# Kernel optimization log

Hardware: AMD Instinct MI355X
Metric: run time of the kernel (lower is better)

Reference implementation:

```python
import jax, jax.numpy as jnp
import numpy as np

DIM = 192          # out_dim
HEADS = 8          # num_heads (split into 2 branches of 4)
SS = (4, 8)        # split_size
B, HH, WW, CIN = 8, 128, 128, 192


def calc_mask(H, W, wh, ww):
    # Swin-style shift mask for windows of (wh, ww), shift (wh//2, ww//2).
    sh, sw = wh // 2, ww // 2
    h = jnp.arange(H)
    w = jnp.arange(W)
    hreg = (h >= H - wh).astype(jnp.int32) + (h >= H - sh).astype(jnp.int32)
    wreg = (w >= W - ww).astype(jnp.int32) + (w >= W - sw).astype(jnp.int32)
    img = hreg[:, None] * 3 + wreg[None, :]                      # (H, W) region ids
    win = img.reshape(H // wh, wh, W // ww, ww).transpose(0, 2, 1, 3).reshape(-1, wh * ww)
    return jnp.where(win[:, :, None] != win[:, None, :], -100.0, 0.0)  # (nW, N, N)


def window_attention(q, k, v, mask, d, Hsp, Wsp):
    # q,k,v: (B, C, H, W); mask: (u*v, N, N); d heads, window Hsp x Wsp
    Bc, C, H, W = k.shape
    u, vv = H // Hsp, W // Wsp
    c = C // d
    N = Hsp * Wsp
    scale = c ** -0.5

    def v2w(t):  # 'b (d c) (u h) (v w) -> (b u v) d (h w) c'
        return t.reshape(Bc, d, c, u, Hsp, vv, Wsp).transpose(0, 3, 5, 1, 4, 6, 2).reshape(Bc * u * vv, d, N, c)

    qw, kw, vw = v2w(q), v2w(k), v2w(v)
    attn = jnp.einsum('ndic,ndjc->ndij', qw, kw) * scale          # (B*u*v, d, N, N)
    attn = attn.reshape(Bc, u * vv, d, N, N) + mask[None, :, None, :, :]
    a = jax.nn.softmax(attn, axis=-1).reshape(Bc * u * vv, d, N, N)
    o = jnp.einsum('ndij,ndjc->ndic', a, vw)
    # '(b u v) d (h w) c -> b (d c) (u h) (v w)'
    return o.reshape(Bc, u, vv, d, Hsp, Wsp, c).transpose(0, 3, 6, 1, 4, 2, 5).reshape(Bc, C, H, W)


def setup_inputs() -> dict:
    key = jax.random.key(0)
    k0, k1, k2, k3 = jax.random.split(key, 4)
    x = jax.random.normal(k0, (B, HH * WW, CIN), dtype=jnp.float32)
    Wq = jax.random.normal(k1, (CIN, DIM), dtype=jnp.float32) * 0.02
    Wkv = jax.random.normal(k2, (CIN, 2 * DIM), dtype=jnp.float32) * 0.02
    Wproj = jax.random.normal(k3, (DIM, DIM), dtype=jnp.float32) * 0.02
    bproj = jnp.zeros((DIM,), dtype=jnp.float32)
    return {"x": x, "Wq": Wq, "Wkv": Wkv, "Wproj": Wproj, "bproj": bproj, "H": HH, "W": WW}


def reference(x, Wq, Wkv, Wproj, bproj, H, W):
    Bc, L, _ = x.shape
    C = Wq.shape[1]
    q = (x @ Wq).reshape(Bc, H, W, C).transpose(0, 3, 1, 2)       # (B, C, H, W)
    kv = (x @ Wkv).reshape(Bc, H, W, 2, C)
    k = kv[..., 0, :].transpose(0, 3, 1, 2)
    v = kv[..., 1, :].transpose(0, 3, 1, 2)

    Ch = C // 2
    s0, s1 = SS[0] // 2, SS[1] // 2
    roll0 = lambda t: jnp.roll(t, (-s0, -s1), axis=(-2, -1))
    roll1 = lambda t: jnp.roll(t, (-s1, -s0), axis=(-2, -1))
    mask0 = calc_mask(H, W, SS[0], SS[1])   # branch 0: 4x8 windows
    mask1 = calc_mask(H, W, SS[1], SS[0])   # branch 1: 8x4 windows
    d = HEADS // 2

    x0 = window_attention(roll0(q[:, :Ch]), roll0(k[:, :Ch]), roll0(v[:, :Ch]), mask0, d, SS[0], SS[1])
    x1 = window_attention(roll1(q[:, Ch:]), roll1(k[:, Ch:]), roll1(v[:, Ch:]), mask1, d, SS[1], SS[0])
    x0 = jnp.roll(x0, (s0, s1), axis=(-2, -1))
    x1 = jnp.roll(x1, (s1, s0), axis=(-2, -1))

    out = jnp.concatenate([x0, x1], axis=1)                        # (B, C, H, W)
    out = out.transpose(0, 2, 3, 1).reshape(Bc, L, C)
    return out @ Wproj + bproj
```

## Files before the change

### kernel.cpp

```cpp
#include <hip/hip_runtime.h>
#include <hip/hip_bf16.h>
#include <stdint.h>

typedef __bf16 bf16;
typedef __bf16 bf16x8 __attribute__((ext_vector_type(8)));
typedef __bf16 bf16x4 __attribute__((ext_vector_type(4)));
typedef float  f32x4  __attribute__((ext_vector_type(4)));

#define MROWS 131072

__device__ __forceinline__ f32x4 mfma16(bf16x8 a, bf16x8 b, f32x4 c) {
    return __builtin_amdgcn_mfma_f32_16x16x32_bf16(a, b, c, 0, 0, 0);
}
__device__ __forceinline__ f32x4 zero4() {
    f32x4 z; z[0]=0.f; z[1]=0.f; z[2]=0.f; z[3]=0.f; return z;
}
__device__ __forceinline__ bf16x8 zero8() {
    bf16x8 z;
#pragma unroll
    for (int i = 0; i < 8; ++i) z[i] = (bf16)0.f;
    return z;
}
template <int CTRL>
__device__ __forceinline__ float rowror(float x) {
    return __int_as_float(
        __builtin_amdgcn_mov_dpp(__float_as_int(x), CTRL, 0xF, 0xF, false));
}
__device__ __forceinline__ float rowmax16(float m) {
    m = fmaxf(m, rowror<0x128>(m));
    m = fmaxf(m, rowror<0x124>(m));
    m = fmaxf(m, rowror<0x122>(m));
    m = fmaxf(m, rowror<0x121>(m));
    return m;
}
__device__ __forceinline__ float rowsum16(float s) {
    s += rowror<0x128>(s);
    s += rowror<0x124>(s);
    s += rowror<0x122>(s);
    s += rowror<0x121>(s);
    return s;
}

__global__ void kw_transpose(const float* __restrict__ Wq, const float* __restrict__ Wkv,
                             const float* __restrict__ Wp, bf16* __restrict__ Wt,
                             bf16* __restrict__ Wpt) {
    int col = blockIdx.x;
    int k = threadIdx.x;
    if (col < 192)      Wt[col * 192 + k] = (bf16)Wq[k * 192 + col];
    else if (col < 576) Wt[col * 192 + k] = (bf16)Wkv[k * 384 + (col - 192)];
    else                Wpt[(col - 576) * 192 + k] = (bf16)Wp[k * 192 + (col - 576)];
}

__global__ __launch_bounds__(256, 4) void kfused(const float* __restrict__ X,
                                                 const bf16* __restrict__ Wt,
                                                 bf16* __restrict__ Out) {
    const int bid = blockIdx.x;
    const int slab = bid & 7;
    const int t = bid >> 3;
    const int img = t >> 7;
    const int idx = t & 127;
    int branch, wa, wb;
    if (idx < 64) {
        branch = 0; wa = slab * 4 + (idx >> 4); wb = idx & 15;
    } else {
        branch = 1; int j = idx - 64; wa = slab * 2 + (j >> 5); wb = j & 31;
    }
    const int wh = branch ? 8 : 4, ww = branch ? 4 : 8;
    const int lww = branch ? 2 : 3;
    const int sh = wh >> 1, sw = ww >> 1;

    __shared__ __align__(16) char smem[31232];
    bf16 (*xs)[200]    = (bf16(*)[200])smem;
    bf16 (*qs)[104]    = (bf16(*)[104])smem;
    bf16 (*ob)[104]    = (bf16(*)[104])smem;
    bf16 (*kss)[104]   = (bf16(*)[104])(smem + 6656);
    bf16 (*pl)[32][40] = (bf16(*)[32][40])(smem + 13312);
    bf16 (*vt)[24][40] = (bf16(*)[24][40])(smem + 23552);
    __shared__ int pix[32];
    __shared__ int rid[32];

    const int tid = threadIdx.x;
    const int hd = tid >> 6;
    const int l = tid & 63, li = l & 15, lk = l >> 4;

    if (tid < 32) {
        int ih = tid >> lww, iw = tid & (ww - 1);
        int hh = wa * wh + ih, wp = wb * ww + iw;
        int hreg = (hh >= 128 - wh) + (hh >= 128 - sh);
        int wreg = (wp >= 128 - ww) + (wp >= 128 - sw);
        rid[tid] = hreg * 3 + wreg;
        int srh = (hh + sh) & 127, srw = (wp + sw) & 127;
        pix[tid] = img * 16384 + srh * 128 + srw;
    }

#pragma unroll
    for (int i = 0; i < 3; ++i) {
        int c = tid + i * 256;
        int row = c / 24, col8 = (c % 24) * 8;
        int ih = row >> lww, iw = row & (ww - 1);
        int hh = wa * wh + ih, wp = wb * ww + iw;
        int srh = (hh + sh) & 127, srw = (wp + sw) & 127;
        const float* p = X + (size_t)(img * 16384 + srh * 128 + srw) * 192 + col8;
        f32x4 f0 = *(const f32x4*)p;
        f32x4 f1 = *(const f32x4*)(p + 4);
        bf16x8 v;
#pragma unroll
        for (int e = 0; e < 4; ++e) { v[e] = (bf16)f0[e]; v[4 + e] = (bf16)f1[e]; }
        *(bf16x8*)&xs[row][col8] = v;
    }
    __syncthreads();

    bf16x8 xf[2][6];
#pragma unroll
    for (int mt = 0; mt < 2; ++mt)
#pragma unroll
        for (int ks = 0; ks < 6; ++ks)
            xf[mt][ks] = *(const bf16x8*)&xs[mt * 16 + li][ks * 32 + lk * 8];

#define LOADW(dst, nt) {                                                            \
        int seg_ = (nt) / 6, cwi_ = ((nt) % 6) * 16;                                \
        const bf16* wr = Wt + (size_t)(seg_ * 192 + branch * 96 + cwi_ + li) * 192  \
                            + lk * 8;                                               \
        _Pragma("unroll")                                                           \
        for (int ks = 0; ks < 6; ++ks) dst[ks] = *(const bf16x8*)(wr + ks * 32);    \
    }
#define MFMA_SCATTER(frag, nt) {                                                    \
        f32x4 a0 = zero4(), a1 = zero4();                                           \
        _Pragma("unroll")                                                           \
        for (int ks = 0; ks < 6; ++ks) {                                            \
            a0 = mfma16(frag[ks], xf[0][ks], a0);                                   \
            a1 = mfma16(frag[ks], xf[1][ks], a1);                                   \
        }                                                                           \
        int seg_ = (nt) / 6, cwi_ = ((nt) % 6) * 16;                                \
        if (seg_ < 2) {                                                             \
            bf16 (*dst)[104] = (seg_ == 0) ? qs : kss;                              \
            bf16x4 p0, p1;                                                          \
            _Pragma("unroll")                                                       \
            for (int r = 0; r < 4; ++r) { p0[r] = (bf16)a0[r]; p1[r] = (bf16)a1[r]; } \
            *(bf16x4*)&dst[li][cwi_ + lk * 4] = p0;                                 \
            *(bf16x4*)&dst[16 + li][cwi_ + lk * 4] = p1;                            \
        } else {                                                                    \
            _Pragma("unroll")                                                       \
            for (int r = 0; r < 4; ++r) {                                           \
                int vc = cwi_ + lk * 4 + r;                                         \
                vt[vc / 24][vc % 24][li] = (bf16)a0[r];                             \
                vt[vc / 24][vc % 24][16 + li] = (bf16)a1[r];                        \
            }                                                                       \
        }                                                                           \
    }

    bf16x8 cur[6], nxt[6];
    LOADW(cur, hd);
    __syncthreads();

#pragma unroll
    for (int j = 0; j < 4; ++j) {
        int nt = hd + 4 * j;
        if (j < 3) {
            LOADW(nxt, nt + 4);
        } else if (hd < 2) {
            LOADW(nxt, nt + 4);
        }
        MFMA_SCATTER(cur, nt);
#pragma unroll
        for (int ks = 0; ks < 6; ++ks) cur[ks] = nxt[ks];
    }
    if (hd < 2) {
        MFMA_SCATTER(cur, hd + 16);
    }
    __syncthreads();

    bf16x8 aq[2], bk[2];
#pragma unroll
    for (int t2 = 0; t2 < 2; ++t2) {
        if (lk < 3) {
            aq[t2] = *(const bf16x8*)&qs[t2 * 16 + li][hd * 24 + lk * 8];
            bk[t2] = *(const bf16x8*)&kss[t2 * 16 + li][hd * 24 + lk * 8];
        } else {
            aq[t2] = zero8();
            bk[t2] = zero8();
        }
    }
    f32x4 s[2][2];
#pragma unroll
    for (int it = 0; it < 2; ++it)
#pragma unroll
        for (int jt = 0; jt < 2; ++jt) s[it][jt] = mfma16(aq[it], bk[jt], zero4());

    const float scale = 0.2041241452319315f;
    const int r0 = lk * 4;
    const int rj0 = rid[li], rj1 = rid[16 + li];
#pragma unroll
    for (int it = 0; it < 2; ++it) {
#pragma unroll
        for (int r = 0; r < 4; ++r) {
            int i = it * 16 + r0 + r;
            int ri = rid[i];
            float v0 = s[it][0][r] * scale + ((ri != rj0) ? -100.f : 0.f);
            float v1 = s[it][1][r] * scale + ((ri != rj1) ? -100.f : 0.f);
            float m = rowmax16(fmaxf(v0, v1));
            float e0 = __expf(v0 - m), e1 = __expf(v1 - m);
            float sm = rowsum16(e0 + e1);
            float inv = 1.f / sm;
            pl[hd][i][li] = (bf16)(e0 * inv);
            pl[hd][i][16 + li] = (bf16)(e1 * inv);
        }
    }
    __syncthreads();

    bf16x8 ap[2], bv[2];
#pragma unroll
    for (int it = 0; it < 2; ++it)
        ap[it] = *(const bf16x8*)&pl[hd][it * 16 + li][lk * 8];
#pragma unroll
    for (int ct = 0; ct < 2; ++ct) {
        int col = ct * 16 + li;
        if (col > 23) col = 23;
        bv[ct] = *(const bf16x8*)&vt[hd][col][lk * 8];
    }
    f32x4 o[2][2];
#pragma unroll
    for (int it = 0; it < 2; ++it)
#pragma unroll
        for (int ct = 0; ct < 2; ++ct) o[it][ct] = mfma16(ap[it], bv[ct], zero4());

#pragma unroll
    for (int it = 0; it < 2; ++it)
#pragma unroll
        for (int ct = 0; ct < 2; ++ct) {
            int col = ct * 16 + li;
            if (col < 24) {
#pragma unroll
                for (int r = 0; r < 4; ++r)
                    ob[it * 16 + r0 + r][hd * 24 + col] = (bf16)o[it][ct][r];
            }
        }
    __syncthreads();
    for (int c = tid; c < 384; c += 256) {
        int row = c / 12, ch = c % 12;
        *(bf16x8*)(Out + (size_t)pix[row] * 192 + branch * 96 + ch * 8) =
            *(const bf16x8*)&ob[row][ch * 8];
    }
#undef LOADW
#undef MFMA_SCATTER
}

#define BSTR 200
__global__ __launch_bounds__(256, 4) void kproj(const bf16* __restrict__ Ab,
                                                const bf16* __restrict__ Wpt,
                                                const float* __restrict__ bias,
                                                float* __restrict__ Out) {
    __shared__ __align__(16) bf16 Bs[96][BSTR];
    const int lid = blockIdx.x;
    const int xcd = lid & 7, s = lid >> 3;
    const int mg = xcd * 128 + s / 2;
    const int nb = s & 1;
    const int tid = threadIdx.x;
    const int w = tid >> 6, l = tid & 63, li = l & 15, lk = l >> 4;
    const int rb = mg * 128 + w * 32;
    const int cb = nb * 96;

    bf16x8 a[2][6];
#pragma unroll
    for (int it = 0; it < 2; ++it)
#pragma unroll
        for (int ks = 0; ks < 6; ++ks)
            a[it][ks] = *(const bf16x8*)(Ab + (size_t)(rb + it * 16 + li) * 192 + ks * 32 + lk * 8);

#pragma unroll
    for (int i = 0; i < 9; ++i) {
        int c = i * 256 + tid;
        int r = c / 24, col = (c % 24) * 8;
        *(bf16x8*)&Bs[r][col] = *(const bf16x8*)(Wpt + (size_t)(cb + r) * 192 + col);
    }
    __syncthreads();

    f32x4 acc[2][6];
#pragma unroll
    for (int it = 0; it < 2; ++it)
#pragma unroll
        for (int nt = 0; nt < 6; ++nt) acc[it][nt] = zero4();

#pragma unroll
    for (int nt = 0; nt < 6; ++nt) {
#pragma unroll
        for (int ks = 0; ks < 6; ++ks) {
            bf16x8 b = *(const bf16x8*)&Bs[nt * 16 + li][ks * 32 + lk * 8];
            acc[0][nt] = mfma16(b, a[0][ks], acc[0][nt]);
            acc[1][nt] = mfma16(b, a[1][ks], acc[1][nt]);
        }
    }

#pragma unroll
    for (int nt = 0; nt < 6; ++nt) {
        f32x4 bv4 = *(const f32x4*)(bias + cb + nt * 16 + lk * 4);
#pragma unroll
        for (int it = 0; it < 2; ++it) {
            f32x4 ov = acc[it][nt];
#pragma unroll
            for (int r = 0; r < 4; ++r) ov[r] += bv4[r];
            *(f32x4*)(Out + (size_t)(rb + it * 16 + li) * 192 + cb + nt * 16 + lk * 4) = ov;
        }
    }
}

extern "C" void kernel_launch(void* const* d_in, const int* in_sizes, int n_in,
                              void* d_out, int out_size, void* d_ws, size_t ws_size,
                              hipStream_t stream) {
    const float* x    = (const float*)d_in[0];
    const float* Wq   = (const float*)d_in[1];
    const float* Wkv  = (const float*)d_in[2];
    const float* Wp   = (const float*)d_in[3];
    const float* bias = (const float*)d_in[4];
    float* out = (float*)d_out;

    bf16* Ab  = (bf16*)d_ws;
    bf16* Wt  = Ab + (size_t)MROWS * 192;
    bf16* Wpt = Wt + 576 * 192;

    hipLaunchKernelGGL(kw_transpose, dim3(768), dim3(192), 0, stream, Wq, Wkv, Wp, Wt, Wpt);
    hipLaunchKernelGGL(kfused, dim3(8192), dim3(256), 0, stream, x, Wt, Ab);
    hipLaunchKernelGGL(kproj, dim3(2048), dim3(256), 0, stream, Ab, Wpt, bias, out);
}
```

Before: 145.7 us.

## Process two windows per block with prefetched second-window inputs and deferred softmax normalization

Each block of the fused QKV+attention kernel now handles two windows instead of one, which halves the grid. The second window's X rows are loaded into registers alongside the first so their global latency overlaps the first window's compute. Softmax no longer subtracts the row max and instead multiplies the output by the reciprocal row sum after the PV MFMA, removing the max reduction. This relies on the logits being small enough not to overflow exp, and it raises register pressure and adds extra barriers per block.

```diff
diff --git a/kernel.cpp b/kernel.cpp
--- a/kernel.cpp
+++ b/kernel.cpp
@@ -25,13 +25,6 @@
 __device__ __forceinline__ float rowror(float x) {
     return __int_as_float(
         __builtin_amdgcn_mov_dpp(__float_as_int(x), CTRL, 0xF, 0xF, false));
-}
-__device__ __forceinline__ float rowmax16(float m) {
-    m = fmaxf(m, rowror<0x128>(m));
-    m = fmaxf(m, rowror<0x124>(m));
-    m = fmaxf(m, rowror<0x122>(m));
-    m = fmaxf(m, rowror<0x121>(m));
-    return m;
 }
 __device__ __forceinline__ float rowsum16(float s) {
     s += rowror<0x128>(s);
@@ -56,18 +49,22 @@
                                                  bf16* __restrict__ Out) {
     const int bid = blockIdx.x;
     const int slab = bid & 7;
-    const int t = bid >> 3;
-    const int img = t >> 7;
-    const int idx = t & 127;
-    int branch, wa, wb;
-    if (idx < 64) {
-        branch = 0; wa = slab * 4 + (idx >> 4); wb = idx & 15;
-    } else {
-        branch = 1; int j = idx - 64; wa = slab * 2 + (j >> 5); wb = j & 31;
-    }
+    const int tt = bid >> 3;
+    const int img = tt >> 6;
+    const int u = tt & 63;
+    const int branch = u >> 5;
+    const int pr = u & 31;
     const int wh = branch ? 8 : 4, ww = branch ? 4 : 8;
     const int lww = branch ? 2 : 3;
     const int sh = wh >> 1, sw = ww >> 1;
+
+    int wa2[2], wb2[2];
+#pragma unroll
+    for (int e = 0; e < 2; ++e) {
+        int qq = 2 * pr + e;
+        wa2[e] = branch ? slab * 2 + (qq >> 5) : slab * 4 + (qq >> 4);
+        wb2[e] = branch ? (qq & 31) : (qq & 15);
+    }
 
     __shared__ __align__(16) char smem[31232];
     bf16 (*xs)[200]    = (bf16(*)[200])smem;
@@ -76,46 +73,53 @@
     bf16 (*kss)[104]   = (bf16(*)[104])(smem + 6656);
     bf16 (*pl)[32][40] = (bf16(*)[32][40])(smem + 13312);
     bf16 (*vt)[24][40] = (bf16(*)[24][40])(smem + 23552);
-    __shared__ int pix[32];
-    __shared__ int rid[32];
+    __shared__ int pix2[2][32];
+    __shared__ int rid2[2][32];
 
     const int tid = threadIdx.x;
     const int hd = tid >> 6;
     const int l = tid & 63, li = l & 15, lk = l >> 4;
 
-    if (tid < 32) {
-        int ih = tid >> lww, iw = tid & (ww - 1);
-        int hh = wa * wh + ih, wp = wb * ww + iw;
+    if (tid < 64) {
+        int e = tid >> 5, tok = tid & 31;
+        int ih = tok >> lww, iw = tok & (ww - 1);
+        int hh = wa2[e] * wh + ih, wp = wb2[e] * ww + iw;
         int hreg = (hh >= 128 - wh) + (hh >= 128 - sh);
         int wreg = (wp >= 128 - ww) + (wp >= 128 - sw);
-        rid[tid] = hreg * 3 + wreg;
+        rid2[e][tok] = hreg * 3 + wreg;
         int srh = (hh + sh) & 127, srw = (wp + sw) & 127;
-        pix[tid] = img * 16384 + srh * 128 + srw;
-    }
-
+        pix2[e][tok] = img * 16384 + srh * 128 + srw;
+    }
+
+    bf16x8 xbr[3];
 #pragma unroll
     for (int i = 0; i < 3; ++i) {
         int c = tid + i * 256;
         int row = c / 24, col8 = (c % 24) * 8;
         int ih = row >> lww, iw = row & (ww - 1);
-        int hh = wa * wh + ih, wp = wb * ww + iw;
-        int srh = (hh + sh) & 127, srw = (wp + sw) & 127;
-        const float* p = X + (size_t)(img * 16384 + srh * 128 + srw) * 192 + col8;
-        f32x4 f0 = *(const f32x4*)p;
-        f32x4 f1 = *(const f32x4*)(p + 4);
-        bf16x8 v;
-#pragma unroll
-        for (int e = 0; e < 4; ++e) { v[e] = (bf16)f0[e]; v[4 + e] = (bf16)f1[e]; }
-        *(bf16x8*)&xs[row][col8] = v;
-    }
-    __syncthreads();
-
-    bf16x8 xf[2][6];
-#pragma unroll
-    for (int mt = 0; mt < 2; ++mt)
-#pragma unroll
-        for (int ks = 0; ks < 6; ++ks)
-            xf[mt][ks] = *(const bf16x8*)&xs[mt * 16 + li][ks * 32 + lk * 8];
+        {
+            int hh = wa2[0] * wh + ih, wp = wb2[0] * ww + iw;
+            int srh = (hh + sh) & 127, srw = (wp + sw) & 127;
+            const float* p = X + (size_t)(img * 16384 + srh * 128 + srw) * 192 + col8;
+            f32x4 f0 = *(const f32x4*)p;
+            f32x4 f1 = *(const f32x4*)(p + 4);
+            bf16x8 v;
+#pragma unroll
+            for (int e2 = 0; e2 < 4; ++e2) { v[e2] = (bf16)f0[e2]; v[4 + e2] = (bf16)f1[e2]; }
+            *(bf16x8*)&xs[row][col8] = v;
+        }
+        {
+            int hh = wa2[1] * wh + ih, wp = wb2[1] * ww + iw;
+            int srh = (hh + sh) & 127, srw = (wp + sw) & 127;
+            const float* p = X + (size_t)(img * 16384 + srh * 128 + srw) * 192 + col8;
+            f32x4 f0 = *(const f32x4*)p;
+            f32x4 f1 = *(const f32x4*)(p + 4);
+            bf16x8 v;
+#pragma unroll
+            for (int e2 = 0; e2 < 4; ++e2) { v[e2] = (bf16)f0[e2]; v[4 + e2] = (bf16)f1[e2]; }
+            xbr[i] = v;
+        }
+    }
 
 #define LOADW(dst, nt) {                                                            \
         int seg_ = (nt) / 6, cwi_ = ((nt) % 6) * 16;                                \
@@ -149,97 +153,121 @@
         }                                                                           \
     }
 
-    bf16x8 cur[6], nxt[6];
-    LOADW(cur, hd);
-    __syncthreads();
-
-#pragma unroll
-    for (int j = 0; j < 4; ++j) {
-        int nt = hd + 4 * j;
-        if (j < 3) {
-            LOADW(nxt, nt + 4);
-        } else if (hd < 2) {
-            LOADW(nxt, nt + 4);
-        }
-        MFMA_SCATTER(cur, nt);
-#pragma unroll
-        for (int ks = 0; ks < 6; ++ks) cur[ks] = nxt[ks];
-    }
-    if (hd < 2) {
-        MFMA_SCATTER(cur, hd + 16);
-    }
-    __syncthreads();
-
-    bf16x8 aq[2], bk[2];
-#pragma unroll
-    for (int t2 = 0; t2 < 2; ++t2) {
-        if (lk < 3) {
-            aq[t2] = *(const bf16x8*)&qs[t2 * 16 + li][hd * 24 + lk * 8];
-            bk[t2] = *(const bf16x8*)&kss[t2 * 16 + li][hd * 24 + lk * 8];
+#pragma unroll
+    for (int win = 0; win < 2; ++win) {
+        if (win == 0) {
+            __syncthreads();
         } else {
-            aq[t2] = zero8();
-            bk[t2] = zero8();
-        }
-    }
-    f32x4 s[2][2];
-#pragma unroll
-    for (int it = 0; it < 2; ++it)
-#pragma unroll
-        for (int jt = 0; jt < 2; ++jt) s[it][jt] = mfma16(aq[it], bk[jt], zero4());
-
-    const float scale = 0.2041241452319315f;
-    const int r0 = lk * 4;
-    const int rj0 = rid[li], rj1 = rid[16 + li];
-#pragma unroll
-    for (int it = 0; it < 2; ++it) {
-#pragma unroll
-        for (int r = 0; r < 4; ++r) {
-            int i = it * 16 + r0 + r;
-            int ri = rid[i];
-            float v0 = s[it][0][r] * scale + ((ri != rj0) ? -100.f : 0.f);
-            float v1 = s[it][1][r] * scale + ((ri != rj1) ? -100.f : 0.f);
-            float m = rowmax16(fmaxf(v0, v1));
-            float e0 = __expf(v0 - m), e1 = __expf(v1 - m);
-            float sm = rowsum16(e0 + e1);
-            float inv = 1.f / sm;
-            pl[hd][i][li] = (bf16)(e0 * inv);
-            pl[hd][i][16 + li] = (bf16)(e1 * inv);
-        }
-    }
-    __syncthreads();
-
-    bf16x8 ap[2], bv[2];
-#pragma unroll
-    for (int it = 0; it < 2; ++it)
-        ap[it] = *(const bf16x8*)&pl[hd][it * 16 + li][lk * 8];
-#pragma unroll
-    for (int ct = 0; ct < 2; ++ct) {
-        int col = ct * 16 + li;
-        if (col > 23) col = 23;
-        bv[ct] = *(const bf16x8*)&vt[hd][col][lk * 8];
-    }
-    f32x4 o[2][2];
-#pragma unroll
-    for (int it = 0; it < 2; ++it)
-#pragma unroll
-        for (int ct = 0; ct < 2; ++ct) o[it][ct] = mfma16(ap[it], bv[ct], zero4());
-
-#pragma unroll
-    for (int it = 0; it < 2; ++it)
+            __syncthreads();
+#pragma unroll
+            for (int i = 0; i < 3; ++i) {
+                int c = tid + i * 256;
+                int row = c / 24, col8 = (c % 24) * 8;
+                *(bf16x8*)&xs[row][col8] = xbr[i];
+            }
+            __syncthreads();
+        }
+
+        bf16x8 xf[2][6];
+#pragma unroll
+        for (int mt = 0; mt < 2; ++mt)
+#pragma unroll
+            for (int ks = 0; ks < 6; ++ks)
+                xf[mt][ks] = *(const bf16x8*)&xs[mt * 16 + li][ks * 32 + lk * 8];
+
+        bf16x8 cur[6], nxt[6];
+        LOADW(cur, hd);
+        __syncthreads();
+
+#pragma unroll
+        for (int j = 0; j < 4; ++j) {
+            int nt = hd + 4 * j;
+            if (j < 3) {
+                LOADW(nxt, nt + 4);
+            } else if (hd < 2) {
+                LOADW(nxt, nt + 4);
+            }
+            MFMA_SCATTER(cur, nt);
+#pragma unroll
+            for (int ks = 0; ks < 6; ++ks) cur[ks] = nxt[ks];
+        }
+        if (hd < 2) {
+            MFMA_SCATTER(cur, hd + 16);
+        }
+        __syncthreads();
+
+        bf16x8 aq[2], bk[2];
+#pragma unroll
+        for (int t2 = 0; t2 < 2; ++t2) {
+            if (lk < 3) {
+                aq[t2] = *(const bf16x8*)&qs[t2 * 16 + li][hd * 24 + lk * 8];
+                bk[t2] = *(const bf16x8*)&kss[t2 * 16 + li][hd * 24 + lk * 8];
+            } else {
+                aq[t2] = zero8();
+                bk[t2] = zero8();
+            }
+        }
+        f32x4 s[2][2];
+#pragma unroll
+        for (int it = 0; it < 2; ++it)
+#pragma unroll
+            for (int jt = 0; jt < 2; ++jt) s[it][jt] = mfma16(aq[it], bk[jt], zero4());
+
+        const float scale = 0.2041241452319315f;
+        const int r0 = lk * 4;
+        const int rj0 = rid2[win][li], rj1 = rid2[win][16 + li];
+        float inv_[2][4];
+#pragma unroll
+        for (int it = 0; it < 2; ++it) {
+#pragma unroll
+            for (int r = 0; r < 4; ++r) {
+                int i = it * 16 + r0 + r;
+                int ri = rid2[win][i];
+                float v0 = s[it][0][r] * scale + ((ri != rj0) ? -100.f : 0.f);
+                float v1 = s[it][1][r] * scale + ((ri != rj1) ? -100.f : 0.f);
+                float e0 = __expf(v0), e1 = __expf(v1);
+                pl[hd][i][li] = (bf16)e0;
+                pl[hd][i][16 + li] = (bf16)e1;
+                float sm = rowsum16(e0 + e1);
+                inv_[it][r] = 1.f / sm;
+            }
+        }
+        __syncthreads();
+
+        bf16x8 ap[2], bv[2];
+#pragma unroll
+        for (int it = 0; it < 2; ++it)
+            ap[it] = *(const bf16x8*)&pl[hd][it * 16 + li][lk * 8];
 #pragma unroll
         for (int ct = 0; ct < 2; ++ct) {
             int col = ct * 16 + li;
-            if (col < 24) {
-#pragma unroll
-                for (int r = 0; r < 4; ++r)
-                    ob[it * 16 + r0 + r][hd * 24 + col] = (bf16)o[it][ct][r];
-            }
-        }
-    __syncthreads();
-    for (int c = tid; c < 384; c += 256) {
-        int row = c / 12, ch = c % 12;
-        *(bf16x8*)(Out + (size_t)pix[row] * 192 + branch * 96 + ch * 8) =
-            *(const bf16x8*)&ob[row][ch * 8];
+            if (col > 23) col = 23;
+            bv[ct] = *(const bf16x8*)&vt[hd][col][lk * 8];
+        }
+        f32x4 o[2][2];
+#pragma unroll
+        for (int it = 0; it < 2; ++it)
+#pragma unroll
+            for (int ct = 0; ct < 2; ++ct) o[it][ct] = mfma16(ap[it], bv[ct], zero4());
+
+#pragma unroll
+        for (int it = 0; it < 2; ++it)
+#pragma unroll
+            for (int ct = 0; ct < 2; ++ct) {
+                int col = ct * 16 + li;
+                if (col < 24) {
+#pragma unroll
+                    for (int r = 0; r < 4; ++r)
+                        ob[it * 16 + r0 + r][hd * 24 + col] =
+                            (bf16)(o[it][ct][r] * inv_[it][r]);
+                }
+            }
+        __syncthreads();
+        for (int c = tid; c < 384; c += 256) {
+            int row = c / 12, ch = c % 12;
+            *(bf16x8*)(Out + (size_t)pix2[win][row] * 192 + branch * 96 + ch * 8) =
+                *(const bf16x8*)&ob[row][ch * 8];
+        }
     }
 #undef LOADW
 #undef MFMA_SCATTER
@@ -319,6 +347,6 @@
     bf16* Wpt = Wt + 576 * 192;
 
     hipLaunchKernelGGL(kw_transpose, dim3(768), dim3(192), 0, stream, Wq, Wkv, Wp, Wt, Wpt);
-    hipLaunchKernelGGL(kfused, dim3(8192), dim3(256), 0, stream, x, Wt, Ab);
+    hipLaunchKernelGGL(kfused, dim3(4096), dim3(256), 0, stream, x, Wt, Ab);
     hipLaunchKernelGGL(kproj, dim3(2048), dim3(256), 0, stream, Ab, Wpt, bias, out);
 }
```

Measured after the change: 196.9 us. 35.1% more time.
